# Performance work log

Hardware: AMD Instinct MI355X
Metric: run time of the kernel (lower is better)

## Reference

```python
import jax, jax.numpy as jnp
import numpy as np

N_QUERIES = 2000
N_DOCS = 128
FEATURE_DIM = 220
HIDDEN = 768
N_IDS = 65536


def setup_inputs() -> dict:
    key = jax.random.key(0)
    k1, k2, k3, k4, k5 = jax.random.split(key, 5)
    qid = jax.random.randint(k1, (N_IDS,), 0, N_QUERIES)
    did = jax.random.randint(k2, (N_IDS,), 0, N_DOCS)
    input_feature_id = jnp.stack([qid, did], axis=1).astype(jnp.int64)
    feature_table = jax.random.normal(k3, (N_QUERIES, N_DOCS, FEATURE_DIM), dtype=jnp.float32) * 10.0
    W = jax.random.normal(k4, (HIDDEN, FEATURE_DIM), dtype=jnp.float32) * (1.0 / np.sqrt(FEATURE_DIM))
    b = jax.random.normal(k5, (HIDDEN,), dtype=jnp.float32) * 0.01
    return {"input_feature_id": input_feature_id, "feature_table": feature_table, "W": W, "b": b}


def reference(input_feature_id, feature_table, W, b):
    # fused gather over (query, doc) ids: [N, FEATURE_DIM]
    feat = feature_table[input_feature_id[:, 0], input_feature_id[:, 1]]
    # log-sign transform: log(|x| + 1) * sign(x)
    feature_batch = jnp.log(jnp.abs(feat) + 1.0) * jnp.sign(feat)
    # Linear + ReLU (torch Linear: x @ W^T + b)
    output_embeds = jax.nn.relu(feature_batch @ W.T + b)
    return (output_embeds, feature_batch)
```

## Files before the change

### kernel.cpp

```cpp
#include <hip/hip_runtime.h>
#include <hip/hip_bf16.h>

#define M_TOTAL 65536
#define ND      128
#define FDIM    220
#define KPAD    224
#define HID     768
#define G8      28
#define BSTRIDE 232

using bf16_t = __hip_bfloat16;
using bf16x8 = __attribute__((ext_vector_type(8))) short;
using f32x4  = __attribute__((ext_vector_type(4))) float;

struct __align__(16) bf16v8 { bf16_t v[8]; };

__device__ __forceinline__ float slog(float x) {
  return copysignf(log1pf(fabsf(x)), x);
}

__device__ __forceinline__ float4 slog4(float4 f) {
  float4 y;
  y.x = slog(f.x); y.y = slog(f.y); y.z = slog(f.z); y.w = slog(f.w);
  return y;
}

__device__ __forceinline__ bf16v8 pack8(float4 a, float4 b) {
  bf16v8 h;
  h.v[0] = __float2bfloat16(a.x); h.v[1] = __float2bfloat16(a.y);
  h.v[2] = __float2bfloat16(a.z); h.v[3] = __float2bfloat16(a.w);
  h.v[4] = __float2bfloat16(b.x); h.v[5] = __float2bfloat16(b.y);
  h.v[6] = __float2bfloat16(b.z); h.v[7] = __float2bfloat16(b.w);
  return h;
}

__global__ __launch_bounds__(256) void convert_w_kernel(
    const float* __restrict__ W, bf16_t* __restrict__ Wb)
{
  const int j   = blockIdx.x * 256 + threadIdx.x;
  const int row = j / G8;
  const int g   = j % G8;

  const float* src = W + (size_t)row * FDIM + g * 8;
  const float4 f0 = *(const float4*)src;
  float4 f1;
  if (g < 27) f1 = *(const float4*)(src + 4);
  else        { f1.x = 0.f; f1.y = 0.f; f1.z = 0.f; f1.w = 0.f; }
  *(bf16v8*)(Wb + (size_t)row * KPAD + g * 8) = pack8(f0, f1);
}

__global__ __launch_bounds__(256, 2) void fused_gather_gemm_kernel(
    const int2* __restrict__ ids, const float* __restrict__ table,
    const bf16_t* __restrict__ Wb, const float* __restrict__ bias,
    float* __restrict__ out, float* __restrict__ fb)
{
  __shared__ bf16_t As[128 * BSTRIDE];

  const int tid = threadIdx.x;
  const int bm  = blockIdx.x;

#pragma unroll
  for (int it = 0; it < 14; ++it) {
    const int jj   = it * 256 + tid;
    const int row  = jj / G8;
    const int g    = jj % G8;
    const int grow = bm * 128 + row;
    const int2 p   = ids[grow];
    const float* src = table + ((size_t)p.x * ND + p.y) * FDIM + g * 8;
    float*       dst = fb + (size_t)grow * FDIM + g * 8;

    const float4 y0 = slog4(*(const float4*)src);
    *(float4*)dst = y0;
    float4 y1;
    if (g < 27) {
      y1 = slog4(*(const float4*)(src + 4));
      *(float4*)(dst + 4) = y1;
    } else {
      y1.x = 0.f; y1.y = 0.f; y1.z = 0.f; y1.w = 0.f;
    }
    *(bf16v8*)(As + row * BSTRIDE + g * 8) = pack8(y0, y1);
  }
  __syncthreads();

  const int wave = tid >> 6;
  const int lane = tid & 63;
  const int wm   = wave & 1;
  const int wn   = wave >> 1;
  const int l15  = lane & 15;
  const int q    = lane >> 4;

  bf16x8 af[7][4];
#pragma unroll
  for (int kb = 0; kb < 7; ++kb)
#pragma unroll
    for (int mi = 0; mi < 4; ++mi)
      af[kb][mi] =
          *(const bf16x8*)(As + (wm * 64 + mi * 16 + l15) * BSTRIDE + kb * 32 + q * 8);

  for (int bn = 0; bn < 6; ++bn) {
    f32x4 acc[4][4];
#pragma unroll
    for (int i = 0; i < 4; ++i)
#pragma unroll
      for (int j = 0; j < 4; ++j) acc[i][j] = (f32x4){0.f, 0.f, 0.f, 0.f};

    const bf16_t* Wbase = Wb + (size_t)(bn * 128 + wn * 64 + l15) * KPAD + q * 8;

#pragma unroll
    for (int kb = 0; kb < 7; ++kb) {
      bf16x8 bg[4];
#pragma unroll
      for (int ni = 0; ni < 4; ++ni)
        bg[ni] = *(const bf16x8*)(Wbase + (size_t)ni * 16 * KPAD + kb * 32);
#pragma unroll
      for (int mi = 0; mi < 4; ++mi)
#pragma unroll
        for (int ni = 0; ni < 4; ++ni)
          acc[mi][ni] = __builtin_amdgcn_mfma_f32_16x16x32_bf16(
              af[kb][mi], bg[ni], acc[mi][ni], 0, 0, 0);
    }

    const int col0 = bn * 128 + wn * 64 + l15;
    const int row0 = bm * 128 + wm * 64 + q * 4;
#pragma unroll
    for (int ni = 0; ni < 4; ++ni) {
      const int n    = col0 + ni * 16;
      const float bv = bias[n];
#pragma unroll
      for (int mi = 0; mi < 4; ++mi) {
#pragma unroll
        for (int r = 0; r < 4; ++r) {
          float v = acc[mi][ni][r] + bv;
          out[(size_t)(row0 + mi * 16 + r) * HID + n] = v > 0.f ? v : 0.f;
        }
      }
    }
  }
}

extern "C" void kernel_launch(void* const* d_in, const int* in_sizes, int n_in,
                              void* d_out, int out_size, void* d_ws, size_t ws_size,
                              hipStream_t stream) {
  (void)in_sizes; (void)n_in; (void)out_size; (void)ws_size;

  const int2*  ids   = (const int2*)d_in[0];
  const float* table = (const float*)d_in[1];
  const float* W     = (const float*)d_in[2];
  const float* bias  = (const float*)d_in[3];

  float* out_embeds = (float*)d_out;
  float* fb_f32     = (float*)d_out + (size_t)M_TOTAL * HID;

  bf16_t* Wb = (bf16_t*)d_ws;

  convert_w_kernel<<<(HID * G8) / 256, 256, 0, stream>>>(W, Wb);

  fused_gather_gemm_kernel<<<M_TOTAL / 128, 256, 0, stream>>>(
      ids, table, Wb, bias, out_embeds, fb_f32);
}
```

Before: 426.1 us.

## Load A fragments directly from global into registers, drop LDS staging, nontemporal stores

```diff
diff --git a/kernel.cpp b/kernel.cpp
--- a/kernel.cpp
+++ b/kernel.cpp
@@ -7,7 +7,6 @@
 #define KPAD    224
 #define HID     768
 #define G8      28
-#define BSTRIDE 232
 
 using bf16_t = __hip_bfloat16;
 using bf16x8 = __attribute__((ext_vector_type(8))) short;
@@ -19,19 +18,19 @@
   return copysignf(log1pf(fabsf(x)), x);
 }
 
-__device__ __forceinline__ float4 slog4(float4 f) {
-  float4 y;
-  y.x = slog(f.x); y.y = slog(f.y); y.z = slog(f.z); y.w = slog(f.w);
+__device__ __forceinline__ f32x4 slog4(f32x4 f) {
+  f32x4 y;
+  y[0] = slog(f[0]); y[1] = slog(f[1]); y[2] = slog(f[2]); y[3] = slog(f[3]);
   return y;
 }
 
-__device__ __forceinline__ bf16v8 pack8(float4 a, float4 b) {
+__device__ __forceinline__ bf16x8 pack8(f32x4 a, f32x4 b) {
   bf16v8 h;
-  h.v[0] = __float2bfloat16(a.x); h.v[1] = __float2bfloat16(a.y);
-  h.v[2] = __float2bfloat16(a.z); h.v[3] = __float2bfloat16(a.w);
-  h.v[4] = __float2bfloat16(b.x); h.v[5] = __float2bfloat16(b.y);
-  h.v[6] = __float2bfloat16(b.z); h.v[7] = __float2bfloat16(b.w);
-  return h;
+  h.v[0] = __float2bfloat16(a[0]); h.v[1] = __float2bfloat16(a[1]);
+  h.v[2] = __float2bfloat16(a[2]); h.v[3] = __float2bfloat16(a[3]);
+  h.v[4] = __float2bfloat16(b[0]); h.v[5] = __float2bfloat16(b[1]);
+  h.v[6] = __float2bfloat16(b[2]); h.v[7] = __float2bfloat16(b[3]);
+  return __builtin_bit_cast(bf16x8, h);
 }
 
 __global__ __launch_bounds__(256) void convert_w_kernel(
@@ -42,11 +41,11 @@
   const int g   = j % G8;
 
   const float* src = W + (size_t)row * FDIM + g * 8;
-  const float4 f0 = *(const float4*)src;
-  float4 f1;
-  if (g < 27) f1 = *(const float4*)(src + 4);
-  else        { f1.x = 0.f; f1.y = 0.f; f1.z = 0.f; f1.w = 0.f; }
-  *(bf16v8*)(Wb + (size_t)row * KPAD + g * 8) = pack8(f0, f1);
+  const f32x4 f0 = *(const f32x4*)src;
+  f32x4 f1;
+  if (g < 27) f1 = *(const f32x4*)(src + 4);
+  else        { f1[0] = 0.f; f1[1] = 0.f; f1[2] = 0.f; f1[3] = 0.f; }
+  *(bf16v8*)(Wb + (size_t)row * KPAD + g * 8) = __builtin_bit_cast(bf16v8, pack8(f0, f1));
 }
 
 __global__ __launch_bounds__(256, 2) void fused_gather_gemm_kernel(
@@ -54,84 +53,79 @@
     const bf16_t* __restrict__ Wb, const float* __restrict__ bias,
     float* __restrict__ out, float* __restrict__ fb)
 {
-  __shared__ bf16_t As[128 * BSTRIDE];
-
-  const int tid = threadIdx.x;
-  const int bm  = blockIdx.x;
-
-#pragma unroll
-  for (int it = 0; it < 14; ++it) {
-    const int jj   = it * 256 + tid;
-    const int row  = jj / G8;
-    const int g    = jj % G8;
-    const int grow = bm * 128 + row;
-    const int2 p   = ids[grow];
-    const float* src = table + ((size_t)p.x * ND + p.y) * FDIM + g * 8;
-    float*       dst = fb + (size_t)grow * FDIM + g * 8;
-
-    const float4 y0 = slog4(*(const float4*)src);
-    *(float4*)dst = y0;
-    float4 y1;
-    if (g < 27) {
-      y1 = slog4(*(const float4*)(src + 4));
-      *(float4*)(dst + 4) = y1;
-    } else {
-      y1.x = 0.f; y1.y = 0.f; y1.z = 0.f; y1.w = 0.f;
-    }
-    *(bf16v8*)(As + row * BSTRIDE + g * 8) = pack8(y0, y1);
-  }
-  __syncthreads();
-
+  const int tid  = threadIdx.x;
+  const int bm   = blockIdx.x;
   const int wave = tid >> 6;
   const int lane = tid & 63;
-  const int wm   = wave & 1;
-  const int wn   = wave >> 1;
   const int l15  = lane & 15;
   const int q    = lane >> 4;
 
-  bf16x8 af[7][4];
+  const int rbase = bm * 128 + wave * 32;
+
+  bf16x8 af[7][2];
 #pragma unroll
-  for (int kb = 0; kb < 7; ++kb)
+  for (int mi = 0; mi < 2; ++mi) {
+    const int grow = rbase + mi * 16 + l15;
+    const int2 p   = ids[grow];
+    const float* srow = table + ((size_t)p.x * ND + p.y) * FDIM;
+    float*       frow = fb + (size_t)grow * FDIM;
 #pragma unroll
-    for (int mi = 0; mi < 4; ++mi)
-      af[kb][mi] =
-          *(const bf16x8*)(As + (wm * 64 + mi * 16 + l15) * BSTRIDE + kb * 32 + q * 8);
+    for (int kb = 0; kb < 7; ++kb) {
+      const int  c0   = kb * 32 + q * 8;
+      const bool tail = (kb == 6) && (q == 3);
+      f32x4 lo = *(const f32x4*)(srow + c0);
+      f32x4 hi;
+      if (!tail) hi = *(const f32x4*)(srow + c0 + 4);
+      else       { hi[0] = 0.f; hi[1] = 0.f; hi[2] = 0.f; hi[3] = 0.f; }
+      lo = slog4(lo);
+      hi = slog4(hi);
+      __builtin_nontemporal_store(lo, (f32x4*)(frow + c0));
+      if (!tail)
+        __builtin_nontemporal_store(hi, (f32x4*)(frow + c0 + 4));
+      af[kb][mi] = pack8(lo, hi);
+    }
+  }
 
   for (int bn = 0; bn < 6; ++bn) {
-    f32x4 acc[4][4];
+    f32x4 acc[2][8];
 #pragma unroll
-    for (int i = 0; i < 4; ++i)
+    for (int i = 0; i < 2; ++i)
 #pragma unroll
-      for (int j = 0; j < 4; ++j) acc[i][j] = (f32x4){0.f, 0.f, 0.f, 0.f};
+      for (int j = 0; j < 8; ++j) acc[i][j] = (f32x4){0.f, 0.f, 0.f, 0.f};
 
-    const bf16_t* Wbase = Wb + (size_t)(bn * 128 + wn * 64 + l15) * KPAD + q * 8;
+    const bf16_t* Wbase = Wb + (size_t)(bn * 128 + l15) * KPAD + q * 8;
 
 #pragma unroll
     for (int kb = 0; kb < 7; ++kb) {
-      bf16x8 bg[4];
+      bf16x8 bg[8];
 #pragma unroll
-      for (int ni = 0; ni < 4; ++ni)
+      for (int ni = 0; ni < 8; ++ni)
         bg[ni] = *(const bf16x8*)(Wbase + (size_t)ni * 16 * KPAD + kb * 32);
 #pragma unroll
-      for (int mi = 0; mi < 4; ++mi)
+      for (int mi = 0; mi < 2; ++mi)
 #pragma unroll
-        for (int ni = 0; ni < 4; ++ni)
+        for (int ni = 0; ni < 8; ++ni)
           acc[mi][ni] = __builtin_amdgcn_mfma_f32_16x16x32_bf16(
               af[kb][mi], bg[ni], acc[mi][ni], 0, 0, 0);
     }
 
-    const int col0 = bn * 128 + wn * 64 + l15;
-    const int row0 = bm * 128 + wm * 64 + q * 4;
+    const int col0 = bn * 128 + l15;
+    const int row0 = rbase + q * 4;
+
+    float bv[8];
 #pragma unroll
-    for (int ni = 0; ni < 4; ++ni) {
-      const int n    = col0 + ni * 16;
-      const float bv = bias[n];
+    for (int ni = 0; ni < 8; ++ni) bv[ni] = bias[col0 + ni * 16];
+
 #pragma unroll
-      for (int mi = 0; mi < 4; ++mi) {
+    for (int mi = 0; mi < 2; ++mi) {
 #pragma unroll
-        for (int r = 0; r < 4; ++r) {
-          float v = acc[mi][ni][r] + bv;
-          out[(size_t)(row0 + mi * 16 + r) * HID + n] = v > 0.f ? v : 0.f;
+      for (int r = 0; r < 4; ++r) {
+        const size_t rowoff = (size_t)(row0 + mi * 16 + r) * HID;
+#pragma unroll
+        for (int ni = 0; ni < 8; ++ni) {
+          float v = acc[mi][ni][r] + bv[ni];
+          v = v > 0.f ? v : 0.f;
+          __builtin_nontemporal_store(v, out + rowoff + col0 + ni * 16);
         }
       }
     }
```

After: 458.6 us. +7.6%, slower.

## Halve row tile, swap MFMA operands for vectorized stores, raise occupancy

Applied to the files above, without the earlier changes.

```diff
diff --git a/kernel.cpp b/kernel.cpp
--- a/kernel.cpp
+++ b/kernel.cpp
@@ -7,6 +7,7 @@
 #define KPAD    224
 #define HID     768
 #define G8      28
+#define BM      64
 #define BSTRIDE 232
 
 using bf16_t = __hip_bfloat16;
@@ -19,19 +20,19 @@
   return copysignf(log1pf(fabsf(x)), x);
 }
 
-__device__ __forceinline__ float4 slog4(float4 f) {
-  float4 y;
-  y.x = slog(f.x); y.y = slog(f.y); y.z = slog(f.z); y.w = slog(f.w);
+__device__ __forceinline__ f32x4 slog4(f32x4 f) {
+  f32x4 y;
+  y[0] = slog(f[0]); y[1] = slog(f[1]); y[2] = slog(f[2]); y[3] = slog(f[3]);
   return y;
 }
 
-__device__ __forceinline__ bf16v8 pack8(float4 a, float4 b) {
+__device__ __forceinline__ bf16x8 pack8(f32x4 a, f32x4 b) {
   bf16v8 h;
-  h.v[0] = __float2bfloat16(a.x); h.v[1] = __float2bfloat16(a.y);
-  h.v[2] = __float2bfloat16(a.z); h.v[3] = __float2bfloat16(a.w);
-  h.v[4] = __float2bfloat16(b.x); h.v[5] = __float2bfloat16(b.y);
-  h.v[6] = __float2bfloat16(b.z); h.v[7] = __float2bfloat16(b.w);
-  return h;
+  h.v[0] = __float2bfloat16(a[0]); h.v[1] = __float2bfloat16(a[1]);
+  h.v[2] = __float2bfloat16(a[2]); h.v[3] = __float2bfloat16(a[3]);
+  h.v[4] = __float2bfloat16(b[0]); h.v[5] = __float2bfloat16(b[1]);
+  h.v[6] = __float2bfloat16(b[2]); h.v[7] = __float2bfloat16(b[3]);
+  return __builtin_bit_cast(bf16x8, h);
 }
 
 __global__ __launch_bounds__(256) void convert_w_kernel(
@@ -42,97 +43,94 @@
   const int g   = j % G8;
 
   const float* src = W + (size_t)row * FDIM + g * 8;
-  const float4 f0 = *(const float4*)src;
-  float4 f1;
-  if (g < 27) f1 = *(const float4*)(src + 4);
-  else        { f1.x = 0.f; f1.y = 0.f; f1.z = 0.f; f1.w = 0.f; }
-  *(bf16v8*)(Wb + (size_t)row * KPAD + g * 8) = pack8(f0, f1);
+  const f32x4 f0 = *(const f32x4*)src;
+  f32x4 f1;
+  if (g < 27) f1 = *(const f32x4*)(src + 4);
+  else        { f1[0] = 0.f; f1[1] = 0.f; f1[2] = 0.f; f1[3] = 0.f; }
+  *(bf16v8*)(Wb + (size_t)row * KPAD + g * 8) = __builtin_bit_cast(bf16v8, pack8(f0, f1));
 }
 
-__global__ __launch_bounds__(256, 2) void fused_gather_gemm_kernel(
+__global__ __launch_bounds__(256, 4) void fused_gather_gemm_kernel(
     const int2* __restrict__ ids, const float* __restrict__ table,
     const bf16_t* __restrict__ Wb, const float* __restrict__ bias,
     float* __restrict__ out, float* __restrict__ fb)
 {
-  __shared__ bf16_t As[128 * BSTRIDE];
+  __shared__ bf16_t As[BM * BSTRIDE];
 
-  const int tid = threadIdx.x;
-  const int bm  = blockIdx.x;
+  const int tid   = threadIdx.x;
+  const int bm    = blockIdx.x;
+  const int rbase = bm * BM;
 
 #pragma unroll
-  for (int it = 0; it < 14; ++it) {
+  for (int it = 0; it < 7; ++it) {
     const int jj   = it * 256 + tid;
     const int row  = jj / G8;
     const int g    = jj % G8;
-    const int grow = bm * 128 + row;
+    const int grow = rbase + row;
     const int2 p   = ids[grow];
     const float* src = table + ((size_t)p.x * ND + p.y) * FDIM + g * 8;
     float*       dst = fb + (size_t)grow * FDIM + g * 8;
 
-    const float4 y0 = slog4(*(const float4*)src);
-    *(float4*)dst = y0;
-    float4 y1;
+    const f32x4 y0 = slog4(*(const f32x4*)src);
+    *(f32x4*)dst = y0;
+    f32x4 y1;
     if (g < 27) {
-      y1 = slog4(*(const float4*)(src + 4));
-      *(float4*)(dst + 4) = y1;
+      y1 = slog4(*(const f32x4*)(src + 4));
+      *(f32x4*)(dst + 4) = y1;
     } else {
-      y1.x = 0.f; y1.y = 0.f; y1.z = 0.f; y1.w = 0.f;
+      y1[0] = 0.f; y1[1] = 0.f; y1[2] = 0.f; y1[3] = 0.f;
     }
-    *(bf16v8*)(As + row * BSTRIDE + g * 8) = pack8(y0, y1);
+    *(bf16v8*)(As + row * BSTRIDE + g * 8) = __builtin_bit_cast(bf16v8, pack8(y0, y1));
   }
   __syncthreads();
 
   const int wave = tid >> 6;
   const int lane = tid & 63;
-  const int wm   = wave & 1;
-  const int wn   = wave >> 1;
   const int l15  = lane & 15;
   const int q    = lane >> 4;
+  const int wn0  = wave * 192;
 
-  bf16x8 af[7][4];
-#pragma unroll
-  for (int kb = 0; kb < 7; ++kb)
-#pragma unroll
-    for (int mi = 0; mi < 4; ++mi)
-      af[kb][mi] =
-          *(const bf16x8*)(As + (wm * 64 + mi * 16 + l15) * BSTRIDE + kb * 32 + q * 8);
-
-  for (int bn = 0; bn < 6; ++bn) {
+  for (int nt = 0; nt < 3; ++nt) {
+    const int n0 = wn0 + nt * 64;
     f32x4 acc[4][4];
 #pragma unroll
     for (int i = 0; i < 4; ++i)
 #pragma unroll
       for (int j = 0; j < 4; ++j) acc[i][j] = (f32x4){0.f, 0.f, 0.f, 0.f};
 
-    const bf16_t* Wbase = Wb + (size_t)(bn * 128 + wn * 64 + l15) * KPAD + q * 8;
+    const bf16_t* Wbase = Wb + (size_t)(n0 + l15) * KPAD + q * 8;
 
 #pragma unroll
     for (int kb = 0; kb < 7; ++kb) {
+      bf16x8 af[4];
+#pragma unroll
+      for (int mi = 0; mi < 4; ++mi)
+        af[mi] = *(const bf16x8*)(As + (mi * 16 + l15) * BSTRIDE + kb * 32 + q * 8);
       bf16x8 bg[4];
 #pragma unroll
       for (int ni = 0; ni < 4; ++ni)
-        bg[ni] = *(const bf16x8*)(Wbase + (size_t)ni * 16 * KPAD + kb * 32);
+        bg[ni] = *(const bf16x8*)(Wbase + (size_t)(ni * 16) * KPAD + kb * 32);
 #pragma unroll
       for (int mi = 0; mi < 4; ++mi)
 #pragma unroll
         for (int ni = 0; ni < 4; ++ni)
           acc[mi][ni] = __builtin_amdgcn_mfma_f32_16x16x32_bf16(
-              af[kb][mi], bg[ni], acc[mi][ni], 0, 0, 0);
+              bg[ni], af[mi], acc[mi][ni], 0, 0, 0);
     }
 
-    const int col0 = bn * 128 + wn * 64 + l15;
-    const int row0 = bm * 128 + wm * 64 + q * 4;
 #pragma unroll
     for (int ni = 0; ni < 4; ++ni) {
-      const int n    = col0 + ni * 16;
-      const float bv = bias[n];
+      const int ncol = n0 + ni * 16 + q * 4;
+      f32x4 bv = *(const f32x4*)(bias + ncol);
 #pragma unroll
       for (int mi = 0; mi < 4; ++mi) {
-#pragma unroll
-        for (int r = 0; r < 4; ++r) {
-          float v = acc[mi][ni][r] + bv;
-          out[(size_t)(row0 + mi * 16 + r) * HID + n] = v > 0.f ? v : 0.f;
-        }
+        f32x4 v = acc[mi][ni];
+        v[0] += bv[0]; v[1] += bv[1]; v[2] += bv[2]; v[3] += bv[3];
+        v[0] = v[0] > 0.f ? v[0] : 0.f;
+        v[1] = v[1] > 0.f ? v[1] : 0.f;
+        v[2] = v[2] > 0.f ? v[2] : 0.f;
+        v[3] = v[3] > 0.f ? v[3] : 0.f;
+        *(f32x4*)(out + (size_t)(rbase + mi * 16 + l15) * HID + ncol) = v;
       }
     }
   }
@@ -155,6 +153,6 @@
 
   convert_w_kernel<<<(HID * G8) / 256, 256, 0, stream>>>(W, Wb);
 
-  fused_gather_gemm_kernel<<<M_TOTAL / 128, 256, 0, stream>>>(
+  fused_gather_gemm_kernel<<<M_TOTAL / BM, 256, 0, stream>>>(
       ids, table, Wb, bias, out_embeds, fb_f32);
 }
```

After: 501.3 us. 17.7% more time.
